# Kernel tuning notes

Measured on AMD Instinct MI355X. Metric: run time of the kernel, lower is better.

Reference implementation:

```python
import jax, jax.numpy as jnp
import numpy as np
from math import sqrt

FMAP = [38, 19, 10, 5, 3, 1]
SCALES = [0.1, 0.2, 0.375, 0.55, 0.725, 0.9]
RATIOS = [[1.0, 2.0, 0.5], [1.0, 2.0, 3.0, 0.5, 0.333], [1.0, 2.0, 3.0, 0.5, 0.333],
          [1.0, 2.0, 3.0, 0.5, 0.333], [1.0, 2.0, 0.5], [1.0, 2.0, 0.5]]
MIN_SCORE = 0.01
MAX_OVERLAP = 0.45
PRE_NMS = 400  # fixed per-class candidate cap (makes NMS jit-compatible)


def make_priors():
    boxes = []
    for k, (fd, s, rs) in enumerate(zip(FMAP, SCALES, RATIOS)):
        for i in range(fd):
            for j in range(fd):
                cx = (j + 0.5) / fd
                cy = (i + 0.5) / fd
                for r in rs:
                    boxes.append([cx, cy, s * sqrt(r), s / sqrt(r)])
                    if r == 1:
                        add = sqrt(s * SCALES[k + 1]) if k + 1 < len(SCALES) else 1.0
                        boxes.append([cx, cy, add, add])
    return np.clip(np.asarray(boxes, np.float32), 0.0, 1.0)  # [8732, 4] cxcywh


def box_iou(a, b):
    # a: [M,4], b: [N,4] in xyxy -> [M,N]
    lt = jnp.maximum(a[:, None, :2], b[None, :, :2])
    rb = jnp.minimum(a[:, None, 2:], b[None, :, 2:])
    wh = jnp.clip(rb - lt, 0.0)
    inter = wh[..., 0] * wh[..., 1]
    area_a = (a[:, 2] - a[:, 0]) * (a[:, 3] - a[:, 1])
    area_b = (b[:, 2] - b[:, 0]) * (b[:, 3] - b[:, 1])
    union = area_a[:, None] + area_b[None, :] - inter
    return inter / jnp.maximum(union, 1e-10)


def _nms_one_class(boxes, scores):
    # boxes: [P,4] xyxy, scores: [P]
    s = jnp.where(scores > MIN_SCORE, scores, -1.0)
    vals, idx = jax.lax.top_k(s, PRE_NMS)          # [PRE]
    cand = boxes[idx]                               # [PRE,4]
    valid = vals > MIN_SCORE
    iou = box_iou(cand, cand)                       # [PRE,PRE]

    def step(sup, i):
        active = valid[i] & ~sup[i]
        new = jnp.where(active, sup | (iou[i] > MAX_OVERLAP), sup)
        new = new.at[i].set(jnp.where(active, False, new[i]))
        return new, None

    sup, _ = jax.lax.scan(step, jnp.zeros(PRE_NMS, bool), jnp.arange(PRE_NMS))
    keep = valid & ~sup
    return cand, jnp.where(keep, vals, -1.0)


def _detect_image(locs, scores, priors, top_k):
    # decode gcxgcy -> cxcywh -> xyxy
    cxcy = locs[:, :2] * priors[:, 2:] / 10.0 + priors[:, :2]
    wh = jnp.exp(locs[:, 2:] / 5.0) * priors[:, 2:]
    boxes = jnp.concatenate([cxcy - wh / 2.0, cxcy + wh / 2.0], axis=-1)  # [P,4]
    probs = jax.nn.softmax(scores, axis=-1)        # [P,C]
    cls_scores = probs[:, 1:].T                     # [C-1, P] (skip background)
    cand_boxes, cand_scores = jax.vmap(lambda s: _nms_one_class(boxes, s))(cls_scores)
    labels = jnp.broadcast_to(jnp.arange(1, probs.shape[1], dtype=jnp.int32)[:, None],
                              cand_scores.shape)
    flat_s = cand_scores.reshape(-1)
    flat_b = cand_boxes.reshape(-1, 4)
    flat_l = labels.reshape(-1)
    top_s, top_i = jax.lax.top_k(flat_s, top_k)
    return flat_b[top_i], flat_l[top_i], top_s


def setup_inputs() -> dict:
    key = jax.random.key(0)
    k1, k2 = jax.random.split(key)
    B, P, C = 8, 8732, 81
    return {
        "predicted_locs": jax.random.normal(k1, (B, P, 4), jnp.float32),
        "predicted_scores": jax.random.normal(k2, (B, P, C), jnp.float32),
        "priors": jnp.asarray(make_priors()),
        "top_k": 200,
    }


def reference(predicted_locs, predicted_scores, priors, top_k):
    # boxes [B,top_k,4], labels [B,top_k] int32, scores [B,top_k]
    # (invalid/padded detections carry score == -1.0)
    return jax.vmap(lambda l, s: _detect_image(l, s, priors, top_k))(
        predicted_locs, predicted_scores)
```

## Files before the change

### kernel.cpp

```cpp
#include <hip/hip_runtime.h>
#include <cstdint>

typedef unsigned long long u64;
typedef unsigned int u32;

#define WPRE 400
#define MIN_SCORE 0.01f
#define MAX_OVERLAP 0.45f
#define INV32 0x407FFFFFu

#define IOU_MID 0x1.CCCCCDp-2

__device__ __forceinline__ u32 f32_key(float f) {
    u32 u = __float_as_uint(f);
    return (f >= 0.0f) ? (u | 0x80000000u) : ~u;
}
__device__ __forceinline__ float key_f32(u32 k) {
    return __uint_as_float((k & 0x80000000u) ? (k ^ 0x80000000u) : ~k);
}

struct SelSt {
    u64 prefix, thr;
    int r, above, shift, nge, done;
    u32 wtot[8];
};

template <int T, typename KF>
__device__ void hist_select64(KF kf, int N, int K, int CAP, u64 bulk,
                              int tid, u32* hist, SelSt* st)
{
    const int lane = tid & 63;
    const int wv = tid >> 6;
    const int nw = T >> 6;
    constexpr int BPT = 1024 / T;

    if (tid == 0) { st->prefix = 0ull; st->r = K; st->above = 0; st->shift = 54; st->done = 0; }
    __syncthreads();

    while (true) {
        const int shift = st->shift;
        const u64 pref = st->prefix;
        const int r = st->r;
        const int above = st->above;
        const bool lvl0 = (shift == 54);
        #pragma unroll
        for (int q = 0; q < BPT; ++q) hist[tid * BPT + q] = 0u;
        __syncthreads();

        const bool useBulk = (bulk != 0ull) && (shift >= 14);
        const u64 bulkHi = bulk >> 14;
        u32 bulkCnt = 0;
        for (int i = tid; i < N; i += T) {
            u64 k;
            if (!kf(i, k)) continue;
            if (!lvl0 && (k >> (shift + 10)) != pref) continue;
            if (useBulk && (k >> 14) == bulkHi) { ++bulkCnt; continue; }
            atomicAdd(&hist[(u32)(k >> shift) & 1023u], 1u);
        }
        if (useBulk) {
            #pragma unroll
            for (int off = 32; off > 0; off >>= 1) bulkCnt += __shfl_down(bulkCnt, off, 64);
            if (lane == 0 && bulkCnt) atomicAdd(&hist[(u32)(bulk >> shift) & 1023u], bulkCnt);
        }
        __syncthreads();

        u32 hloc[BPT], Sarr[BPT];
        u32 run = 0;
        #pragma unroll
        for (int q = BPT - 1; q >= 0; --q) {
            hloc[q] = hist[tid * BPT + q];
            run += hloc[q];
            Sarr[q] = run;
        }
        u32 incl = run;
        #pragma unroll
        for (int off = 1; off < 64; off <<= 1) {
            u32 x = __shfl_down(incl, off, 64);
            incl += (lane + off < 64) ? x : 0u;
        }
        if (lane == 0) st->wtot[wv] = incl;
        __syncthreads();
        u32 wa = 0;
        for (int w2 = wv + 1; w2 < nw; ++w2) wa += st->wtot[w2];
        const u32 suffAbove = wa + (incl - run);

        bool found = false; int fb = 0; u32 fSn = 0, fh = 0;
        #pragma unroll
        for (int q = 0; q < BPT; ++q) {
            u32 S = suffAbove + Sarr[q];
            u32 Sn = S - hloc[q];
            if ((int)S >= r && (int)Sn < r) { found = true; fb = tid * BPT + q; fSn = Sn; fh = hloc[q]; }
        }
        __syncthreads();
        if (found) {
            u64 np = (pref << 10) | (u64)(u32)fb;
            int nab = above + (int)fSn;
            int nge = nab + (int)fh;
            st->prefix = np;
            st->r = r - (int)fSn;
            st->above = nab;
            st->nge = nge;
            st->thr = np << shift;
            st->shift = shift - 10;
            st->done = (nge <= CAP) || (shift == 4);
        }
        __syncthreads();
        if (st->done) break;
    }
}

__global__ __launch_bounds__(256) void decode_softmax_kernel(
    const float* __restrict__ locs, const float* __restrict__ scores,
    const float* __restrict__ priors, float* __restrict__ dec,
    float* __restrict__ probs_t, int P, int C, int NC)
{
    __shared__ float tile[64 * 81];
    __shared__ float mrow[64], srow[64];
    const int b  = blockIdx.y;
    const int p0 = blockIdx.x * 64;
    const int tid = threadIdx.x;
    const int nrows = min(64, P - p0);
    const int n = nrows * C;

    const float* src = scores + ((size_t)b * P + p0) * C;
    for (int idx = tid; idx < n; idx += 256) tile[idx] = src[idx];

    if (tid < nrows) {
        int p = p0 + tid;
        float4 lc = ((const float4*)locs)[(size_t)b * P + p];
        float4 pr = ((const float4*)priors)[p];
        float cx = lc.x * pr.z / 10.0f + pr.x;
        float cy = lc.y * pr.w / 10.0f + pr.y;
        float w  = expf(lc.z / 5.0f) * pr.z;
        float h  = expf(lc.w / 5.0f) * pr.w;
        ((float4*)dec)[(size_t)b * P + p] =
            make_float4(cx - w * 0.5f, cy - h * 0.5f, cx + w * 0.5f, cy + h * 0.5f);
    }
    __syncthreads();

    if (tid < nrows) {
        const float* row = &tile[tid * C];
        float m = row[0];
        for (int cc = 1; cc < C; ++cc) m = fmaxf(m, row[cc]);
        float ss = 0.f;
        for (int cc = 0; cc < C; ++cc) ss += expf(row[cc] - m);
        mrow[tid] = m; srow[tid] = ss;
    }
    __syncthreads();

    for (int idx = tid; idx < 64 * NC; idx += 256) {
        int r  = idx & 63;
        int cc = idx >> 6;
        if (r < nrows) {
            float v = expf(tile[r * C + cc + 1] - mrow[r]) / srow[r];
            probs_t[((size_t)(b * NC + cc)) * P + p0 + r] = v;
        }
    }
}

__global__ __launch_bounds__(512) void select_nms_kernel(
    const float* __restrict__ dec, const float* __restrict__ probs_t,
    float* __restrict__ cand_sc, float* __restrict__ cand_bx,
    int P, int NC)
{
    const int c = blockIdx.x, b = blockIdx.y;
    const int tid = threadIdx.x;
    const int lane = tid & 63;
    const int wv = tid >> 6;
    const int T = 512;

    __shared__ alignas(16) char bufA[8736 * 4];
    u32* skey = (u32*)bufA;
    u64* inw  = (u64*)bufA;
    float4* cbox = (float4*)(bufA + 25088);
    __shared__ u64 cand[512];
    u32* hist = (u32*)cand;
    __shared__ u64 validm[7], keepm[7];
    __shared__ SelSt st;
    __shared__ int sh_cnt;

    const float* ps = probs_t + ((size_t)(b * NC + c)) * P;

    int P4 = P >> 2;
    for (int i = tid; i < P4; i += T) {
        float4 f4 = ((const float4*)ps)[i];
        skey[i*4+0] = f32_key(f4.x > MIN_SCORE ? f4.x : -1.0f);
        skey[i*4+1] = f32_key(f4.y > MIN_SCORE ? f4.y : -1.0f);
        skey[i*4+2] = f32_key(f4.z > MIN_SCORE ? f4.z : -1.0f);
        skey[i*4+3] = f32_key(f4.w > MIN_SCORE ? f4.w : -1.0f);
    }
    for (int i = (P4 << 2) + tid; i < P; i += T) {
        float f = ps[i];
        skey[i] = f32_key(f > MIN_SCORE ? f : -1.0f);
    }
    if (tid == 0) sh_cnt = 0;
    __syncthreads();

    hist_select64<512>([&](int i, u64& k) {
                           k = ((u64)skey[i] << 32) | (u64)(u32)(~(u32)i);
                           return true;
                       },
                       P, WPRE, 512, (((u64)INV32) << 32) | 0xFFFFFFFFull,
                       tid, hist, &st);
    const u64 thr = st.thr;

    for (int i = tid; i < P; i += T) {
        u64 k = ((u64)skey[i] << 32) | (u64)(u32)(~(u32)i);
        if (k >= thr) {
            int pos = atomicAdd(&sh_cnt, 1);
            if (pos < 512) cand[pos] = k;
        }
    }
    __syncthreads();
    const int cnt = sh_cnt;
    u64 v = (tid < cnt) ? cand[tid] : 0ull;

    for (int k = 2; k <= 512; k <<= 1) {
        for (int j = k >> 1; j > 0; j >>= 1) {
            u64 p;
            if (j < 64) {
                p = __shfl_xor(v, j, 64);
            } else {
                __syncthreads();
                cand[tid] = v;
                __syncthreads();
                p = cand[tid ^ j];
            }
            bool takeMax = (((tid & k) == 0) == ((tid & j) == 0));
            v = takeMax ? (v > p ? v : p) : (v > p ? p : v);
        }
    }
    __syncthreads();

    float4 mybox = make_float4(0.f, 0.f, 0.f, 0.f);
    float myval = -1.0f;
    if (tid < 448) {
        if (tid < WPRE) {
            myval = key_f32((u32)(v >> 32));
            int p = (int)(~(u32)v);
            mybox = ((const float4*)dec)[(size_t)b * P + p];
        }
        cbox[tid] = mybox;
        u64 mk = __ballot(myval > MIN_SCORE);
        if (lane == 0) validm[tid >> 6] = mk;
    }
    __syncthreads();

    for (int tt = wv; tt < 28; tt += 8) {
        int r = 0, base = 0;
        while (tt - base >= 7 - r) { base += 7 - r; ++r; }
        int w = r + (tt - base);
        int j = (w << 6) + lane;
        float4 bj = cbox[j];
        float aj = (bj.z - bj.x) * (bj.w - bj.y);
        const int i0 = r << 6;
        u32 acc0 = 0u, acc1 = 0u;
        #pragma unroll 16
        for (int q = 0; q < 32; ++q) {
            int i = i0 + q;
            float4 bi = cbox[i];
            float ai = (bi.z - bi.x) * (bi.w - bi.y);
            float lx = fmaxf(bi.x, bj.x);
            float ly = fmaxf(bi.y, bj.y);
            float rx = fminf(bi.z, bj.z);
            float ry = fminf(bi.w, bj.w);
            float ww = fmaxf(rx - lx, 0.f);
            float hh = fmaxf(ry - ly, 0.f);
            float inter = ww * hh;
            float uniC = fmaxf((ai + aj) - inter, 1e-10f);
            bool pred = (double)inter > IOU_MID * (double)uniC;
            acc0 |= pred ? (1u << q) : 0u;
        }
        #pragma unroll 16
        for (int q = 0; q < 32; ++q) {
            int i = i0 + 32 + q;
            float4 bi = cbox[i];
            float ai = (bi.z - bi.x) * (bi.w - bi.y);
            float lx = fmaxf(bi.x, bj.x);
            float ly = fmaxf(bi.y, bj.y);
            float rx = fminf(bi.z, bj.z);
            float ry = fminf(bi.w, bj.w);
            float ww = fmaxf(rx - lx, 0.f);
            float hh = fmaxf(ry - ly, 0.f);
            float inter = ww * hh;
            float uniC = fmaxf((ai + aj) - inter, 1e-10f);
            bool pred = (double)inter > IOU_MID * (double)uniC;
            acc1 |= pred ? (1u << q) : 0u;
        }
        inw[(w * 7 + r) * 64 + lane] = ((u64)acc1 << 32) | acc0;
    }
    __syncthreads();

    if (wv == 0) {
        u64 keep[7];
        #pragma unroll
        for (int w2 = 0; w2 < 7; ++w2) {
            bool alive = ((validm[w2] >> lane) & 1ull) != 0;
            #pragma unroll
            for (int r = 0; r < w2; ++r) {
                u64 inr = inw[(w2 * 7 + r) * 64 + lane];
                alive = alive && ((inr & keep[r]) == 0ull);
            }
            u64 in_self = inw[(w2 * 7 + w2) * 64 + lane];
            u64 inmask = in_self & ((1ull << lane) - 1ull);
            u64 mm = inmask;
            #pragma unroll
            for (int off = 32; off; off >>= 1) mm |= __shfl_xor(mm, off, 64);
            while (mm) {
                int t = __builtin_ctzll(mm);
                mm &= mm - 1ull;
                u64 am = __ballot(alive);
                if ((am >> t) & 1ull)
                    alive = alive && (((inmask >> t) & 1ull) == 0ull);
            }
            u64 fin = __ballot(alive);
            keep[w2] = fin;
            if (lane == 0) keepm[w2] = fin;
        }
    }
    __syncthreads();

    if (tid < WPRE) {
        bool keep = (keepm[tid >> 6] >> (tid & 63)) & 1ull;
        cand_sc[((size_t)(b * NC + c)) * WPRE + tid] = keep ? myval : -1.0f;
        ((float4*)cand_bx)[((size_t)(b * NC + c)) * WPRE + tid] = mybox;
    }
}

__global__ __launch_bounds__(512) void topkA_kernel(
    const float* __restrict__ cand_sc, u64* __restrict__ wsA,
    int NC, int TOPK, int GS, int NG)
{
    const int g = blockIdx.x, b = blockIdx.y;
    const int tid = threadIdx.x;
    const int T = 512;
    const int N = GS;
    const u32 fbase = (u32)(g * GS);

    __shared__ u32 hist[1024];
    __shared__ SelSt st;
    __shared__ int sh_cnt;

    const float* s = cand_sc + (size_t)b * NC * WPRE + (size_t)g * GS;
    u64* outg = wsA + (size_t)(b * NG + g) * 256;

    if (tid == 0) sh_cnt = 0;
    __syncthreads();

    hist_select64<512>([&](int i, u64& k) {
                           k = ((u64)f32_key(s[i]) << 32) | (u64)(u32)(~(fbase + (u32)i));
                           return true;
                       },
                       N, TOPK, 256,
                       (((u64)INV32) << 32) | (u64)(u32)(~fbase),
                       tid, hist, &st);
    const u64 thr = st.thr;

    for (int i = tid; i < N; i += T) {
        u64 k = ((u64)f32_key(s[i]) << 32) | (u64)(u32)(~(fbase + (u32)i));
        if (k >= thr) {
            int pos = atomicAdd(&sh_cnt, 1);
            if (pos < 256) outg[pos] = k;
        }
    }
    __syncthreads();
    int cnt = sh_cnt;
    if (tid < 256 && tid >= cnt) outg[tid] = 0ull;
}

__global__ __launch_bounds__(256) void topkB_kernel(
    const u64* __restrict__ wsA, const float* __restrict__ cand_bx,
    float* __restrict__ out, int NC, int TOPK, int B, int NG)
{
    const int b = blockIdx.x;
    const int tid = threadIdx.x;
    const int T = 256;
    const int N = NG * 256;

    __shared__ u64 keys[2560];
    __shared__ u32 hist[1024];
    u64* cand = (u64*)hist;
    __shared__ SelSt st;
    __shared__ int sh_cnt;

    const u64* src = wsA + (size_t)b * N;
    for (int i = tid; i < N; i += T) keys[i] = src[i];
    if (tid == 0) sh_cnt = 0;
    __syncthreads();

    hist_select64<256>([&](int i, u64& k) { k = keys[i]; return true; },
                       N, TOPK, 256, (((u64)INV32) << 32) | 0xFFFFFFFFull,
                       tid, hist, &st);
    const u64 thr = st.thr;

    for (int i = tid; i < N; i += T) {
        u64 k = keys[i];
        if (k >= thr) {
            int pos = atomicAdd(&sh_cnt, 1);
            if (pos < 256) cand[pos] = k;
        }
    }
    __syncthreads();
    int cnt = sh_cnt;
    u64 v = (tid < cnt) ? cand[tid] : 0ull;

    for (int k = 2; k <= 256; k <<= 1) {
        for (int j = k >> 1; j > 0; j >>= 1) {
            u64 p;
            if (j < 64) {
                p = __shfl_xor(v, j, 64);
            } else {
                __syncthreads();
                cand[tid] = v;
                __syncthreads();
                p = cand[tid ^ j];
            }
            bool takeMax = (((tid & k) == 0) == ((tid & j) == 0));
            v = takeMax ? (v > p ? v : p) : (v > p ? p : v);
        }
    }

    if (tid < TOPK) {
        float sc = key_f32((u32)(v >> 32));
        int flat = (int)(~(u32)v);
        int cls = flat / WPRE;
        float4 bx = ((const float4*)cand_bx)[(size_t)b * NC * WPRE + flat];
        float* ob = out + ((size_t)(b * TOPK + tid)) * 4;
        ob[0] = bx.x; ob[1] = bx.y; ob[2] = bx.z; ob[3] = bx.w;
        out[(size_t)B * TOPK * 4 + (size_t)b * TOPK + tid] = (float)(cls + 1);
        out[(size_t)B * TOPK * 5 + (size_t)b * TOPK + tid] = sc;
    }
}

extern "C" void kernel_launch(void* const* d_in, const int* in_sizes, int n_in,
                              void* d_out, int out_size, void* d_ws, size_t ws_size,
                              hipStream_t stream) {
    const float* locs   = (const float*)d_in[0];
    const float* scores = (const float*)d_in[1];
    const float* priors = (const float*)d_in[2];

    const int P  = in_sizes[2] / 4;
    const int B  = in_sizes[0] / (4 * P);
    const int C  = in_sizes[1] / (B * P);
    const int NC = C - 1;
    const int TOPK = out_size / (B * 6);
    const int NG = 10;
    const int GS = (NC * WPRE) / NG;

    float* ws      = (float*)d_ws;
    float* dec     = ws;
    float* probs_t = dec + (size_t)B * P * 4;
    float* cand_sc = probs_t + (size_t)B * NC * P;
    float* cand_bx = cand_sc + (size_t)B * NC * WPRE;
    u64*   wsA     = (u64*)(cand_bx + (size_t)B * NC * WPRE * 4);

    dim3 g1((P + 63) / 64, B);
    decode_softmax_kernel<<<g1, 256, 0, stream>>>(locs, scores, priors, dec, probs_t, P, C, NC);

    dim3 g2(NC, B);
    select_nms_kernel<<<g2, 512, 0, stream>>>(dec, probs_t, cand_sc, cand_bx, P, NC);

    dim3 g3(NG, B);
    topkA_kernel<<<g3, 512, 0, stream>>>(cand_sc, wsA, NC, TOPK, GS, NG);
    topkB_kernel<<<dim3(B), 256, 0, stream>>>(wsA, cand_bx, (float*)d_out, NC, TOPK, B, NG);
}
```

Baseline: 131.2 us.

## Fuse two-stage top-k into a single 1024-thread per-image selection kernel

Replaces the grouped top-k pass (10 blocks per image writing 256 candidates each to a workspace) and the second merge kernel with one 1024-thread block per image. That block radix-selects directly over all 32000 candidate scores and then bitonic-sorts the top 256. A new select variant buckets every key whose score equals the invalid sentinel, so the many -1 entries skip the histogram atomics. This removes one launch and the workspace round-trip, at the cost of only 8 blocks of parallelism, each making several passes over 32000 global scores.

```diff
diff --git a/kernel.cpp b/kernel.cpp
--- a/kernel.cpp
+++ b/kernel.cpp
@@ -22,7 +22,7 @@
 struct SelSt {
     u64 prefix, thr;
     int r, above, shift, nge, done;
-    u32 wtot[8];
+    u32 wtot[16];
 };
 
 template <int T, typename KF>
@@ -58,6 +58,89 @@
             atomicAdd(&hist[(u32)(k >> shift) & 1023u], 1u);
         }
         if (useBulk) {
+            #pragma unroll
+            for (int off = 32; off > 0; off >>= 1) bulkCnt += __shfl_down(bulkCnt, off, 64);
+            if (lane == 0 && bulkCnt) atomicAdd(&hist[(u32)(bulk >> shift) & 1023u], bulkCnt);
+        }
+        __syncthreads();
+
+        u32 hloc[BPT], Sarr[BPT];
+        u32 run = 0;
+        #pragma unroll
+        for (int q = BPT - 1; q >= 0; --q) {
+            hloc[q] = hist[tid * BPT + q];
+            run += hloc[q];
+            Sarr[q] = run;
+        }
+        u32 incl = run;
+        #pragma unroll
+        for (int off = 1; off < 64; off <<= 1) {
+            u32 x = __shfl_down(incl, off, 64);
+            incl += (lane + off < 64) ? x : 0u;
+        }
+        if (lane == 0) st->wtot[wv] = incl;
+        __syncthreads();
+        u32 wa = 0;
+        for (int w2 = wv + 1; w2 < nw; ++w2) wa += st->wtot[w2];
+        const u32 suffAbove = wa + (incl - run);
+
+        bool found = false; int fb = 0; u32 fSn = 0, fh = 0;
+        #pragma unroll
+        for (int q = 0; q < BPT; ++q) {
+            u32 S = suffAbove + Sarr[q];
+            u32 Sn = S - hloc[q];
+            if ((int)S >= r && (int)Sn < r) { found = true; fb = tid * BPT + q; fSn = Sn; fh = hloc[q]; }
+        }
+        __syncthreads();
+        if (found) {
+            u64 np = (pref << 10) | (u64)(u32)fb;
+            int nab = above + (int)fSn;
+            int nge = nab + (int)fh;
+            st->prefix = np;
+            st->r = r - (int)fSn;
+            st->above = nab;
+            st->nge = nge;
+            st->thr = np << shift;
+            st->shift = shift - 10;
+            st->done = (nge <= CAP) || (shift == 4);
+        }
+        __syncthreads();
+        if (st->done) break;
+    }
+}
+
+template <int T, typename KF>
+__device__ void hist_select64_sc(KF kf, int N, int K, int CAP, u64 bulk,
+                                 int tid, u32* hist, SelSt* st)
+{
+    const int lane = tid & 63;
+    const int wv = tid >> 6;
+    const int nw = T >> 6;
+    constexpr int BPT = 1024 / T;
+    const u32 bulkScore = (u32)(bulk >> 32);
+
+    if (tid == 0) { st->prefix = 0ull; st->r = K; st->above = 0; st->shift = 54; st->done = 0; }
+    __syncthreads();
+
+    while (true) {
+        const int shift = st->shift;
+        const u64 pref = st->prefix;
+        const int r = st->r;
+        const int above = st->above;
+        const bool lvl0 = (shift == 54);
+        #pragma unroll
+        for (int q = 0; q < BPT; ++q) hist[tid * BPT + q] = 0u;
+        __syncthreads();
+
+        u32 bulkCnt = 0;
+        for (int i = tid; i < N; i += T) {
+            u64 k;
+            if (!kf(i, k)) continue;
+            if (!lvl0 && (k >> (shift + 10)) != pref) continue;
+            if ((u32)(k >> 32) == bulkScore) { ++bulkCnt; continue; }
+            atomicAdd(&hist[(u32)(k >> shift) & 1023u], 1u);
+        }
+        {
             #pragma unroll
             for (int off = 32; off > 0; off >>= 1) bulkCnt += __shfl_down(bulkCnt, off, 64);
             if (lane == 0 && bulkCnt) atomicAdd(&hist[(u32)(bulk >> shift) & 1023u], bulkCnt);
@@ -327,74 +410,34 @@
     }
 }
 
-__global__ __launch_bounds__(512) void topkA_kernel(
-    const float* __restrict__ cand_sc, u64* __restrict__ wsA,
-    int NC, int TOPK, int GS, int NG)
-{
-    const int g = blockIdx.x, b = blockIdx.y;
-    const int tid = threadIdx.x;
-    const int T = 512;
-    const int N = GS;
-    const u32 fbase = (u32)(g * GS);
-
-    __shared__ u32 hist[1024];
-    __shared__ SelSt st;
-    __shared__ int sh_cnt;
-
-    const float* s = cand_sc + (size_t)b * NC * WPRE + (size_t)g * GS;
-    u64* outg = wsA + (size_t)(b * NG + g) * 256;
-
-    if (tid == 0) sh_cnt = 0;
-    __syncthreads();
-
-    hist_select64<512>([&](int i, u64& k) {
-                           k = ((u64)f32_key(s[i]) << 32) | (u64)(u32)(~(fbase + (u32)i));
-                           return true;
-                       },
-                       N, TOPK, 256,
-                       (((u64)INV32) << 32) | (u64)(u32)(~fbase),
-                       tid, hist, &st);
-    const u64 thr = st.thr;
-
-    for (int i = tid; i < N; i += T) {
-        u64 k = ((u64)f32_key(s[i]) << 32) | (u64)(u32)(~(fbase + (u32)i));
-        if (k >= thr) {
-            int pos = atomicAdd(&sh_cnt, 1);
-            if (pos < 256) outg[pos] = k;
-        }
-    }
-    __syncthreads();
-    int cnt = sh_cnt;
-    if (tid < 256 && tid >= cnt) outg[tid] = 0ull;
-}
-
-__global__ __launch_bounds__(256) void topkB_kernel(
-    const u64* __restrict__ wsA, const float* __restrict__ cand_bx,
-    float* __restrict__ out, int NC, int TOPK, int B, int NG)
+__global__ __launch_bounds__(1024) void topk_fused_kernel(
+    const float* __restrict__ cand_sc, const float* __restrict__ cand_bx,
+    float* __restrict__ out, int NC, int TOPK, int B)
 {
     const int b = blockIdx.x;
     const int tid = threadIdx.x;
-    const int T = 256;
-    const int N = NG * 256;
-
-    __shared__ u64 keys[2560];
+    const int T = 1024;
+    const int N = NC * WPRE;
+
     __shared__ u32 hist[1024];
-    u64* cand = (u64*)hist;
+    __shared__ u64 cand[256];
     __shared__ SelSt st;
     __shared__ int sh_cnt;
 
-    const u64* src = wsA + (size_t)b * N;
-    for (int i = tid; i < N; i += T) keys[i] = src[i];
+    const float* s = cand_sc + (size_t)b * N;
     if (tid == 0) sh_cnt = 0;
     __syncthreads();
 
-    hist_select64<256>([&](int i, u64& k) { k = keys[i]; return true; },
-                       N, TOPK, 256, (((u64)INV32) << 32) | 0xFFFFFFFFull,
-                       tid, hist, &st);
+    hist_select64_sc<1024>([&](int i, u64& k) {
+                               k = ((u64)f32_key(s[i]) << 32) | (u64)(u32)(~(u32)i);
+                               return true;
+                           },
+                           N, TOPK, 256, (((u64)INV32) << 32) | 0xFFFFFFFFull,
+                           tid, hist, &st);
     const u64 thr = st.thr;
 
     for (int i = tid; i < N; i += T) {
-        u64 k = keys[i];
+        u64 k = ((u64)f32_key(s[i]) << 32) | (u64)(u32)(~(u32)i);
         if (k >= thr) {
             int pos = atomicAdd(&sh_cnt, 1);
             if (pos < 256) cand[pos] = k;
@@ -402,7 +445,7 @@
     }
     __syncthreads();
     int cnt = sh_cnt;
-    u64 v = (tid < cnt) ? cand[tid] : 0ull;
+    u64 v = (tid < 256 && tid < cnt) ? cand[tid] : 0ull;
 
     for (int k = 2; k <= 256; k <<= 1) {
         for (int j = k >> 1; j > 0; j >>= 1) {
@@ -411,9 +454,9 @@
                 p = __shfl_xor(v, j, 64);
             } else {
                 __syncthreads();
-                cand[tid] = v;
+                if (tid < 256) cand[tid] = v;
                 __syncthreads();
-                p = cand[tid ^ j];
+                p = (tid < 256) ? cand[tid ^ j] : 0ull;
             }
             bool takeMax = (((tid & k) == 0) == ((tid & j) == 0));
             v = takeMax ? (v > p ? v : p) : (v > p ? p : v);
@@ -424,7 +467,7 @@
         float sc = key_f32((u32)(v >> 32));
         int flat = (int)(~(u32)v);
         int cls = flat / WPRE;
-        float4 bx = ((const float4*)cand_bx)[(size_t)b * NC * WPRE + flat];
+        float4 bx = ((const float4*)cand_bx)[(size_t)b * N + flat];
         float* ob = out + ((size_t)(b * TOPK + tid)) * 4;
         ob[0] = bx.x; ob[1] = bx.y; ob[2] = bx.z; ob[3] = bx.w;
         out[(size_t)B * TOPK * 4 + (size_t)b * TOPK + tid] = (float)(cls + 1);
@@ -444,15 +487,12 @@
     const int C  = in_sizes[1] / (B * P);
     const int NC = C - 1;
     const int TOPK = out_size / (B * 6);
-    const int NG = 10;
-    const int GS = (NC * WPRE) / NG;
 
     float* ws      = (float*)d_ws;
     float* dec     = ws;
     float* probs_t = dec + (size_t)B * P * 4;
     float* cand_sc = probs_t + (size_t)B * NC * P;
     float* cand_bx = cand_sc + (size_t)B * NC * WPRE;
-    u64*   wsA     = (u64*)(cand_bx + (size_t)B * NC * WPRE * 4);
 
     dim3 g1((P + 63) / 64, B);
     decode_softmax_kernel<<<g1, 256, 0, stream>>>(locs, scores, priors, dec, probs_t, P, C, NC);
@@ -460,7 +500,5 @@
     dim3 g2(NC, B);
     select_nms_kernel<<<g2, 512, 0, stream>>>(dec, probs_t, cand_sc, cand_bx, P, NC);
 
-    dim3 g3(NG, B);
-    topkA_kernel<<<g3, 512, 0, stream>>>(cand_sc, wsA, NC, TOPK, GS, NG);
-    topkB_kernel<<<dim3(B), 256, 0, stream>>>(wsA, cand_bx, (float*)d_out, NC, TOPK, B, NG);
-}
+    topk_fused_kernel<<<dim3(B), 1024, 0, stream>>>(cand_sc, cand_bx, (float*)d_out, NC, TOPK, B);
+}
```

Result: slower. 152.8 us (+16.5%).
